# Performance work log

Measured on AMD Instinct MI355X. Metric: run time of the kernel, lower is better.

## Reference

```python
import jax, jax.numpy as jnp
import numpy as np

N, E, IN, H, C = 20000, 320000, 512, 4, 64
HC = H * C
EPS_BN = 1e-5


def setup_inputs() -> dict:
    key = jax.random.key(0)
    ks = jax.random.split(key, 12)
    p = lambda k, shape, s=0.05: jax.random.normal(k, shape, dtype=jnp.float32) * s
    z = lambda n: jnp.zeros((n,), jnp.float32)
    o = lambda n: jnp.ones((n,), jnp.float32)
    return {
        "x": jax.random.normal(ks[0], (N, IN), dtype=jnp.float32),
        "edge_index": jax.random.randint(ks[1], (2, E), 0, N),
        "Wl0": p(ks[2], (IN, HC)), "Wr0": p(ks[3], (IN, HC)),
        "att0": p(ks[4], (H, C)), "b0": z(HC),
        "g0": o(HC), "be0": z(HC), "m0": z(HC), "v0": o(HC),
        "Wl1": p(ks[5], (HC, HC)), "Wr1": p(ks[6], (HC, HC)),
        "att1": p(ks[7], (H, C)), "b1": z(HC),
        "g1": o(HC), "be1": z(HC), "m1": z(HC), "v1": o(HC),
        "Wl2": p(ks[8], (HC, 2)), "Wr2": p(ks[9], (HC, 2)),
        "att2": p(ks[10], (1, 2)), "b2": z(2),
    }


def gatv2_conv(x, Wl, Wr, att, b, ei, concat):
    # GATv2: e_ij = att . LeakyReLU(Wl x_j + Wr x_i); softmax over in-edges of i
    n = x.shape[0]
    h, c = att.shape
    xl = (x @ Wl).reshape(n, h, c)  # source/message transform
    xr = (x @ Wr).reshape(n, h, c)  # target transform
    src, dst = ei[0], ei[1]
    m = xl[src] + xr[dst]                                   # [E,H,C] edge gather
    e = jnp.sum(jax.nn.leaky_relu(m, 0.2) * att, axis=-1)   # [E,H]
    emax = jax.ops.segment_max(e, dst, num_segments=n)      # segment softmax
    emax = jnp.where(jnp.isfinite(emax), emax, 0.0)
    ex = jnp.exp(e - emax[dst])
    denom = jax.ops.segment_sum(ex, dst, num_segments=n)
    alpha = ex / (denom[dst] + 1e-16)                       # [E,H]
    out = jax.ops.segment_sum(alpha[:, :, None] * xl[src], dst, num_segments=n)
    out = out.reshape(n, h * c) if concat else out.mean(axis=1)
    return out + b


def bn_eval(x, g, be, m, v):
    return (x - m) * (g * jax.lax.rsqrt(v + EPS_BN)) + be


def reference(x, edge_index, Wl0, Wr0, att0, b0, g0, be0, m0, v0,
              Wl1, Wr1, att1, b1, g1, be1, m1, v1, Wl2, Wr2, att2, b2):
    loops = jnp.arange(N)
    ei = jnp.concatenate([edge_index, jnp.stack([loops, loops])], axis=1)
    h = gatv2_conv(x, Wl0, Wr0, att0, b0, ei, True)
    h = jax.nn.elu(bn_eval(h, g0, be0, m0, v0))
    h = gatv2_conv(h, Wl1, Wr1, att1, b1, ei, True)
    h = jax.nn.elu(bn_eval(h, g1, be1, m1, v1))
    out = gatv2_conv(h, Wl2, Wr2, att2, b2, ei, False)
    return jax.nn.log_softmax(out, axis=1)
```

## Files before the change

kernel.cpp:

```cpp
#include <hip/hip_runtime.h>
#include <math.h>

#define NN 20000
#define MP 20096
#define EE 320000
#define ET (EE + NN)
#define HC 256
#define EPS_BN 1e-5f

typedef __bf16 bf16x8 __attribute__((ext_vector_type(8)));
typedef float f32x4 __attribute__((ext_vector_type(4)));

__device__ __forceinline__ float4 ld4(const float* p) { return *reinterpret_cast<const float4*>(p); }
__device__ __forceinline__ float lrelu(float x) { return fmaxf(x, 0.f) + 0.2f * fminf(x, 0.f); }

__device__ __forceinline__ unsigned short f2b(float f) {
  unsigned int u = __float_as_uint(f);
  u = (u + 0x7fffu + ((u >> 16) & 1u)) >> 16;
  return (unsigned short)u;
}
__device__ __forceinline__ float b2f(unsigned short u) {
  return __uint_as_float(((unsigned int)u) << 16);
}

__device__ __forceinline__ void gld_lds16(const void* g, void* l) {
  __builtin_amdgcn_global_load_lds(
      (const __attribute__((address_space(1))) unsigned int*)g,
      (__attribute__((address_space(3))) unsigned int*)(unsigned int)(unsigned long long)l,
      16, 0, 0);
}

__global__ __launch_bounds__(256) void convert_x_kernel(const float* __restrict__ x,
                                                        unsigned short* __restrict__ xb) {
  int i = (blockIdx.x * 256 + threadIdx.x) * 4;
  if (i >= NN * 512) return;
  float4 v = ld4(&x[i]);
  ushort4 o;
  o.x = f2b(v.x); o.y = f2b(v.y); o.z = f2b(v.z); o.w = f2b(v.w);
  *reinterpret_cast<ushort4*>(&xb[i]) = o;
}

__global__ __launch_bounds__(256) void convert_w_kernel(const float* __restrict__ Wl,
                                                        const float* __restrict__ Wr,
                                                        unsigned short* __restrict__ Wf,
                                                        int K) {
  int idx = blockIdx.x * 256 + threadIdx.x;
  if (idx >= 512 * K) return;
  int n = idx / K, k = idx - n * K;
  float v = (n < 256) ? Wl[(size_t)k * 256 + n] : Wr[(size_t)k * 256 + (n - 256)];
  Wf[idx] = f2b(v);
}

__global__ __launch_bounds__(256) void gemm_mfma(const unsigned short* __restrict__ A,
                                                 const unsigned short* __restrict__ Bt,
                                                 unsigned short* __restrict__ xlb,
                                                 float* __restrict__ xrf,
                                                 int M, int K) {
  __shared__ unsigned short As[128 * 32];
  __shared__ unsigned short Bs[128 * 32];
  const int wave = threadIdx.x >> 6;
  const int lane = threadIdx.x & 63;
  const int am = lane & 15;
  const int aq = lane >> 4;
  const int wr = (wave >> 1) * 64;
  const int wc = (wave & 1) * 64;
  const int row0 = blockIdx.y * 128;
  const int col0 = blockIdx.x * 128;

  f32x4 acc[4][4] = {};

  for (int kk = 0; kk < K; kk += 32) {
    __syncthreads();
#pragma unroll
    for (int c = 0; c < 2; ++c) {
      int seg = wave * 128 + c * 64 + lane;
      int r = seg >> 2, ks = (seg & 3) * 8;
      gld_lds16(A + (size_t)(row0 + r) * K + kk + ks, &As[(wave * 128 + c * 64) * 8]);
      gld_lds16(Bt + (size_t)(col0 + r) * K + kk + ks, &Bs[(wave * 128 + c * 64) * 8]);
    }
    __syncthreads();

    bf16x8 af[4], bfr[4];
#pragma unroll
    for (int i = 0; i < 4; ++i)
      af[i] = *reinterpret_cast<const bf16x8*>(&As[(wr + i * 16 + am) * 32 + aq * 8]);
#pragma unroll
    for (int j = 0; j < 4; ++j)
      bfr[j] = *reinterpret_cast<const bf16x8*>(&Bs[(wc + j * 16 + am) * 32 + aq * 8]);
#pragma unroll
    for (int i = 0; i < 4; ++i)
#pragma unroll
      for (int j = 0; j < 4; ++j)
        acc[i][j] = __builtin_amdgcn_mfma_f32_16x16x32_bf16(af[i], bfr[j], acc[i][j], 0, 0, 0);
  }

#pragma unroll
  for (int i = 0; i < 4; ++i) {
#pragma unroll
    for (int j = 0; j < 4; ++j) {
      int gcol = col0 + wc + j * 16 + am;
#pragma unroll
      for (int rr = 0; rr < 4; ++rr) {
        int grow = row0 + wr + i * 16 + aq * 4 + rr;
        if (grow < M) {
          float v = acc[i][j][rr];
          if (gcol < 256) xlb[(size_t)grow * 256 + gcol] = f2b(v);
          else            xrf[(size_t)grow * 256 + (gcol - 256)] = v;
        }
      }
    }
  }
}

__global__ __launch_bounds__(256) void hist_kernel(const int* __restrict__ ei,
                                                   int* __restrict__ counts) {
  int e = blockIdx.x * blockDim.x + threadIdx.x;
  if (e >= ET) return;
  int d = (e < EE) ? ei[EE + e] : (e - EE);
  atomicAdd(&counts[d], 1);
}

__global__ __launch_bounds__(1024) void scan_kernel(int* __restrict__ cursor,
                                                    int* __restrict__ offsets) {
  __shared__ int wsum[16];
  const int tid = threadIdx.x;
  const int lane = tid & 63, wv = tid >> 6;
  const int base = tid * 20;
  int vals[20];
  int s = 0;
  if (tid < 1000) {
#pragma unroll
    for (int j = 0; j < 20; ++j) { vals[j] = cursor[base + j]; s += vals[j]; }
  }
  int ssum = s;
#pragma unroll
  for (int off = 1; off < 64; off <<= 1) {
    int t = __shfl_up(ssum, off);
    if (lane >= off) ssum += t;
  }
  if (lane == 63) wsum[wv] = ssum;
  __syncthreads();
  if (wv == 0) {
    int w = (lane < 16) ? wsum[lane] : 0;
#pragma unroll
    for (int off = 1; off < 16; off <<= 1) {
      int t = __shfl_up(w, off);
      if (lane >= off) w += t;
    }
    if (lane < 16) wsum[lane] = w;
  }
  __syncthreads();
  int excl = ssum - s + (wv > 0 ? wsum[wv - 1] : 0);
  if (tid < 1000) {
    int run = excl;
#pragma unroll
    for (int j = 0; j < 20; ++j) { offsets[base + j] = run; cursor[base + j] = run; run += vals[j]; }
  }
  if (tid == 1023) offsets[NN] = wsum[15];
}

__global__ __launch_bounds__(256) void scatter_kernel(const int* __restrict__ ei,
                                                      int* __restrict__ cursor,
                                                      int* __restrict__ srcs) {
  int e = blockIdx.x * blockDim.x + threadIdx.x;
  if (e >= ET) return;
  int s, d;
  if (e < EE) { s = ei[e]; d = ei[EE + e]; } else { s = d = e - EE; }
  int pos = atomicAdd(&cursor[d], 1);
  srcs[pos] = s;
}

__global__ __launch_bounds__(256) void gat_layer(const unsigned short* __restrict__ xlb,
                                                 const float* __restrict__ xrf,
                                                 const float* __restrict__ att,
                                                 const float* __restrict__ bias,
                                                 const float* __restrict__ gam,
                                                 const float* __restrict__ bet,
                                                 const float* __restrict__ mean,
                                                 const float* __restrict__ var,
                                                 const int* __restrict__ offsets,
                                                 const int* __restrict__ srcs,
                                                 unsigned short* __restrict__ hb) {
  const int wave = threadIdx.x >> 6;
  const int lane = threadIdx.x & 63;
  const int node = blockIdx.x * 4 + wave;
  if (node >= NN) return;

  const float4 xr4 = ld4(&xrf[(size_t)node * HC + lane * 4]);
  const float4 a4 = ld4(&att[lane * 4]);
  const int beg = offsets[node];
  const int end = offsets[node + 1];

  float lA = 0.f, lB = 0.f;
  float4 OA = make_float4(0.f, 0.f, 0.f, 0.f);
  float4 OB = make_float4(0.f, 0.f, 0.f, 0.f);

  int i = beg;
  for (; i + 3 < end; i += 4) {
    int s0 = srcs[i], s1 = srcs[i + 1], s2 = srcs[i + 2], s3 = srcs[i + 3];
    ushort4 u0 = *reinterpret_cast<const ushort4*>(&xlb[(size_t)s0 * HC + lane * 4]);
    ushort4 u1 = *reinterpret_cast<const ushort4*>(&xlb[(size_t)s1 * HC + lane * 4]);
    ushort4 u2 = *reinterpret_cast<const ushort4*>(&xlb[(size_t)s2 * HC + lane * 4]);
    ushort4 u3 = *reinterpret_cast<const ushort4*>(&xlb[(size_t)s3 * HC + lane * 4]);
    float4 x0 = make_float4(b2f(u0.x), b2f(u0.y), b2f(u0.z), b2f(u0.w));
    float4 x1 = make_float4(b2f(u1.x), b2f(u1.y), b2f(u1.z), b2f(u1.w));
    float4 x2 = make_float4(b2f(u2.x), b2f(u2.y), b2f(u2.z), b2f(u2.w));
    float4 x3 = make_float4(b2f(u3.x), b2f(u3.y), b2f(u3.z), b2f(u3.w));
    float e0 = lrelu(x0.x + xr4.x) * a4.x + lrelu(x0.y + xr4.y) * a4.y +
               lrelu(x0.z + xr4.z) * a4.z + lrelu(x0.w + xr4.w) * a4.w;
    float e1 = lrelu(x1.x + xr4.x) * a4.x + lrelu(x1.y + xr4.y) * a4.y +
               lrelu(x1.z + xr4.z) * a4.z + lrelu(x1.w + xr4.w) * a4.w;
    float e2 = lrelu(x2.x + xr4.x) * a4.x + lrelu(x2.y + xr4.y) * a4.y +
               lrelu(x2.z + xr4.z) * a4.z + lrelu(x2.w + xr4.w) * a4.w;
    float e3 = lrelu(x3.x + xr4.x) * a4.x + lrelu(x3.y + xr4.y) * a4.y +
               lrelu(x3.z + xr4.z) * a4.z + lrelu(x3.w + xr4.w) * a4.w;
#pragma unroll
    for (int off = 1; off < 16; off <<= 1) {
      e0 += __shfl_xor(e0, off);
      e1 += __shfl_xor(e1, off);
      e2 += __shfl_xor(e2, off);
      e3 += __shfl_xor(e3, off);
    }
    float p0 = __expf(e0), p1 = __expf(e1), p2 = __expf(e2), p3 = __expf(e3);
    lA += p0; lB += p1; lA += p2; lB += p3;
    OA.x += p0 * x0.x; OA.y += p0 * x0.y; OA.z += p0 * x0.z; OA.w += p0 * x0.w;
    OB.x += p1 * x1.x; OB.y += p1 * x1.y; OB.z += p1 * x1.z; OB.w += p1 * x1.w;
    OA.x += p2 * x2.x; OA.y += p2 * x2.y; OA.z += p2 * x2.z; OA.w += p2 * x2.w;
    OB.x += p3 * x3.x; OB.y += p3 * x3.y; OB.z += p3 * x3.z; OB.w += p3 * x3.w;
  }
  for (; i < end; ++i) {
    int s = srcs[i];
    ushort4 u = *reinterpret_cast<const ushort4*>(&xlb[(size_t)s * HC + lane * 4]);
    float4 x0 = make_float4(b2f(u.x), b2f(u.y), b2f(u.z), b2f(u.w));
    float e = lrelu(x0.x + xr4.x) * a4.x + lrelu(x0.y + xr4.y) * a4.y +
              lrelu(x0.z + xr4.z) * a4.z + lrelu(x0.w + xr4.w) * a4.w;
#pragma unroll
    for (int off = 1; off < 16; off <<= 1) e += __shfl_xor(e, off);
    float p = __expf(e);
    lA += p;
    OA.x += p * x0.x; OA.y += p * x0.y; OA.z += p * x0.z; OA.w += p * x0.w;
  }
  float inv = 1.f / (lA + lB);
  float4 O = make_float4(OA.x + OB.x, OA.y + OB.y, OA.z + OB.z, OA.w + OB.w);

  float4 b4 = ld4(&bias[lane * 4]);
  float4 g4 = ld4(&gam[lane * 4]);
  float4 e4 = ld4(&bet[lane * 4]);
  float4 m4 = ld4(&mean[lane * 4]);
  float4 v4 = ld4(&var[lane * 4]);
  float y0 = O.x * inv + b4.x, y1 = O.y * inv + b4.y;
  float y2 = O.z * inv + b4.z, y3 = O.w * inv + b4.w;
  float z0 = (y0 - m4.x) * (g4.x * rsqrtf(v4.x + EPS_BN)) + e4.x;
  float z1 = (y1 - m4.y) * (g4.y * rsqrtf(v4.y + EPS_BN)) + e4.y;
  float z2 = (y2 - m4.z) * (g4.z * rsqrtf(v4.z + EPS_BN)) + e4.z;
  float z3 = (y3 - m4.w) * (g4.w * rsqrtf(v4.w + EPS_BN)) + e4.w;
  ushort4 r;
  r.x = f2b(z0 > 0.f ? z0 : expm1f(z0));
  r.y = f2b(z1 > 0.f ? z1 : expm1f(z1));
  r.z = f2b(z2 > 0.f ? z2 : expm1f(z2));
  r.w = f2b(z3 > 0.f ? z3 : expm1f(z3));
  *reinterpret_cast<ushort4*>(&hb[(size_t)node * HC + lane * 4]) = r;
}

__global__ __launch_bounds__(256) void lin2_kernel(const unsigned short* __restrict__ hb,
                                                   const float* __restrict__ Wl,
                                                   const float* __restrict__ Wr,
                                                   float* __restrict__ xl2,
                                                   float* __restrict__ xr2) {
  const int wave = threadIdx.x >> 6;
  const int lane = threadIdx.x & 63;
  const int node = blockIdx.x * 4 + wave;
  if (node >= NN) return;
  ushort4 h4 = *reinterpret_cast<const ushort4*>(&hb[(size_t)node * HC + lane * 4]);
  float hv[4] = {b2f(h4.x), b2f(h4.y), b2f(h4.z), b2f(h4.w)};
  float l0 = 0.f, l1 = 0.f, r0 = 0.f, r1 = 0.f;
#pragma unroll
  for (int j = 0; j < 4; ++j) {
    int row = lane * 4 + j;
    l0 += hv[j] * Wl[row * 2 + 0];
    l1 += hv[j] * Wl[row * 2 + 1];
    r0 += hv[j] * Wr[row * 2 + 0];
    r1 += hv[j] * Wr[row * 2 + 1];
  }
#pragma unroll
  for (int off = 1; off < 64; off <<= 1) {
    l0 += __shfl_xor(l0, off);
    l1 += __shfl_xor(l1, off);
    r0 += __shfl_xor(r0, off);
    r1 += __shfl_xor(r1, off);
  }
  if (lane == 0) {
    xl2[node * 2 + 0] = l0; xl2[node * 2 + 1] = l1;
    xr2[node * 2 + 0] = r0; xr2[node * 2 + 1] = r1;
  }
}

__global__ __launch_bounds__(256) void gat2_out_kernel(const float* __restrict__ xl2,
                                                       const float* __restrict__ xr2,
                                                       const float* __restrict__ att2,
                                                       const float* __restrict__ b2,
                                                       const int* __restrict__ offsets,
                                                       const int* __restrict__ srcs,
                                                       float* __restrict__ out) {
  const int wave = threadIdx.x >> 6;
  const int lane = threadIdx.x & 63;
  const int node = blockIdx.x * 4 + wave;
  if (node >= NN) return;
  const float a0 = att2[0], a1 = att2[1];
  const float xr0 = xr2[node * 2 + 0], xr1 = xr2[node * 2 + 1];
  const int beg = offsets[node], end = offsets[node + 1];

  float l = 0.f, o0 = 0.f, o1 = 0.f;
  for (int i = beg + lane; i < end; i += 64) {
    int s = srcs[i];
    float x0 = xl2[s * 2 + 0], x1 = xl2[s * 2 + 1];
    float e = lrelu(x0 + xr0) * a0 + lrelu(x1 + xr1) * a1;
    float p = __expf(e);
    l += p;
    o0 += p * x0;
    o1 += p * x1;
  }
#pragma unroll
  for (int off = 1; off < 64; off <<= 1) {
    l += __shfl_xor(l, off);
    o0 += __shfl_xor(o0, off);
    o1 += __shfl_xor(o1, off);
  }
  if (lane == 0) {
    float inv = 1.f / l;
    float t0 = o0 * inv + b2[0];
    float t1 = o1 * inv + b2[1];
    float mx = fmaxf(t0, t1);
    float ls = mx + logf(__expf(t0 - mx) + __expf(t1 - mx));
    out[node * 2 + 0] = t0 - ls;
    out[node * 2 + 1] = t1 - ls;
  }
}

extern "C" void kernel_launch(void* const* d_in, const int* in_sizes, int n_in,
                              void* d_out, int out_size, void* d_ws, size_t ws_size,
                              hipStream_t stream) {
  const float* x    = (const float*)d_in[0];
  const int*   ei   = (const int*)d_in[1];
  const float* Wl0  = (const float*)d_in[2];
  const float* Wr0  = (const float*)d_in[3];
  const float* att0 = (const float*)d_in[4];
  const float* b0   = (const float*)d_in[5];
  const float* g0   = (const float*)d_in[6];
  const float* be0  = (const float*)d_in[7];
  const float* m0   = (const float*)d_in[8];
  const float* v0   = (const float*)d_in[9];
  const float* Wl1  = (const float*)d_in[10];
  const float* Wr1  = (const float*)d_in[11];
  const float* att1 = (const float*)d_in[12];
  const float* b1   = (const float*)d_in[13];
  const float* g1   = (const float*)d_in[14];
  const float* be1  = (const float*)d_in[15];
  const float* m1   = (const float*)d_in[16];
  const float* v1   = (const float*)d_in[17];
  const float* Wl2  = (const float*)d_in[18];
  const float* Wr2  = (const float*)d_in[19];
  const float* att2 = (const float*)d_in[20];
  const float* b2   = (const float*)d_in[21];

  float* xrf = (float*)d_ws;
  unsigned short* xlb = (unsigned short*)(xrf + (size_t)NN * 256);
  unsigned short* hb  = xlb + (size_t)NN * 256;
  unsigned short* xb  = hb + (size_t)MP * 256;
  unsigned short* Wf0 = xb + (size_t)MP * 512;
  unsigned short* Wf1 = Wf0 + 512 * 512;
  float* xl2 = (float*)(Wf1 + 512 * 256);
  float* xr2 = xl2 + 2 * NN;
  int* offsets = (int*)(xr2 + 2 * NN);
  int* cursor  = offsets + (NN + 1);
  int* srcs    = cursor + NN;

  hipMemsetAsync(cursor, 0, NN * sizeof(int), stream);
  hist_kernel<<<(ET + 255) / 256, 256, 0, stream>>>(ei, cursor);
  convert_x_kernel<<<(NN * 512 / 4 + 255) / 256, 256, 0, stream>>>(x, xb);
  convert_w_kernel<<<(512 * 512 + 255) / 256, 256, 0, stream>>>(Wl0, Wr0, Wf0, 512);
  convert_w_kernel<<<(512 * 256 + 255) / 256, 256, 0, stream>>>(Wl1, Wr1, Wf1, 256);
  scan_kernel<<<1, 1024, 0, stream>>>(cursor, offsets);
  scatter_kernel<<<(ET + 255) / 256, 256, 0, stream>>>(ei, cursor, srcs);

  dim3 gemm_grid(4, MP / 128);
  gemm_mfma<<<gemm_grid, 256, 0, stream>>>(xb, Wf0, xlb, xrf, NN, 512);
  gat_layer<<<NN / 4, 256, 0, stream>>>(xlb, xrf, att0, b0, g0, be0, m0, v0, offsets, srcs, hb);
  gemm_mfma<<<gemm_grid, 256, 0, stream>>>(hb, Wf1, xlb, xrf, NN, 256);
  gat_layer<<<NN / 4, 256, 0, stream>>>(xlb, xrf, att1, b1, g1, be1, m1, v1, offsets, srcs, hb);
  lin2_kernel<<<NN / 4, 256, 0, stream>>>(hb, Wl2, Wr2, xl2, xr2);
  gat2_out_kernel<<<NN / 4, 256, 0, stream>>>(xl2, xr2, att2, b2, offsets, srcs, (float*)d_out);
}
```

Before: 301.6 us.

## Fuse prep kernels, split GAT edges across two waves, fuse lin2 into layer1

Merges the x conversion, both weight conversions and the degree histogram into one launch. The GAT layers now assign two waves per node, each handling half the in-edges, and merge partial sums through shared memory. The final projection (lin2) is folded into the second GAT layer's epilogue, so the hidden activations are no longer written out and read back. The aim is fewer launches, more parallelism for latency-bound gathers, and less memory traffic, at the cost of a block barrier and an idle second wave during the epilogue.

```diff
diff --git a/kernel.cpp b/kernel.cpp
--- a/kernel.cpp
+++ b/kernel.cpp
@@ -8,6 +8,12 @@
 #define HC 256
 #define EPS_BN 1e-5f
 
+#define PB_CX 5000
+#define PB_W0 1024
+#define PB_W1 512
+#define PB_HIST 1329
+#define PB_TOTAL (PB_CX + PB_W0 + PB_W1 + PB_HIST)
+
 typedef __bf16 bf16x8 __attribute__((ext_vector_type(8)));
 typedef float f32x4 __attribute__((ext_vector_type(4)));
 
@@ -30,25 +36,44 @@
       16, 0, 0);
 }
 
-__global__ __launch_bounds__(256) void convert_x_kernel(const float* __restrict__ x,
-                                                        unsigned short* __restrict__ xb) {
-  int i = (blockIdx.x * 256 + threadIdx.x) * 4;
-  if (i >= NN * 512) return;
-  float4 v = ld4(&x[i]);
-  ushort4 o;
-  o.x = f2b(v.x); o.y = f2b(v.y); o.z = f2b(v.z); o.w = f2b(v.w);
-  *reinterpret_cast<ushort4*>(&xb[i]) = o;
-}
-
-__global__ __launch_bounds__(256) void convert_w_kernel(const float* __restrict__ Wl,
-                                                        const float* __restrict__ Wr,
-                                                        unsigned short* __restrict__ Wf,
-                                                        int K) {
-  int idx = blockIdx.x * 256 + threadIdx.x;
-  if (idx >= 512 * K) return;
-  int n = idx / K, k = idx - n * K;
-  float v = (n < 256) ? Wl[(size_t)k * 256 + n] : Wr[(size_t)k * 256 + (n - 256)];
-  Wf[idx] = f2b(v);
+__global__ __launch_bounds__(256) void prep_kernel(const float* __restrict__ x,
+                                                   unsigned short* __restrict__ xb,
+                                                   const float* __restrict__ Wl0,
+                                                   const float* __restrict__ Wr0,
+                                                   unsigned short* __restrict__ Wf0,
+                                                   const float* __restrict__ Wl1,
+                                                   const float* __restrict__ Wr1,
+                                                   unsigned short* __restrict__ Wf1,
+                                                   const int* __restrict__ ei,
+                                                   int* __restrict__ counts) {
+  const int b = blockIdx.x;
+  const int tid = threadIdx.x;
+  if (b < PB_CX) {
+    int i = (b * 256 + tid) * 8;
+    float4 v0 = ld4(&x[i]);
+    float4 v1 = ld4(&x[i + 4]);
+    ushort4 o0, o1;
+    o0.x = f2b(v0.x); o0.y = f2b(v0.y); o0.z = f2b(v0.z); o0.w = f2b(v0.w);
+    o1.x = f2b(v1.x); o1.y = f2b(v1.y); o1.z = f2b(v1.z); o1.w = f2b(v1.w);
+    *reinterpret_cast<ushort4*>(&xb[i]) = o0;
+    *reinterpret_cast<ushort4*>(&xb[i + 4]) = o1;
+  } else if (b < PB_CX + PB_W0) {
+    int idx = (b - PB_CX) * 256 + tid;
+    int n = idx >> 9, k = idx & 511;
+    float v = (n < 256) ? Wl0[(size_t)k * 256 + n] : Wr0[(size_t)k * 256 + (n - 256)];
+    Wf0[idx] = f2b(v);
+  } else if (b < PB_CX + PB_W0 + PB_W1) {
+    int idx = (b - PB_CX - PB_W0) * 256 + tid;
+    int n = idx >> 8, k = idx & 255;
+    float v = (n < 256) ? Wl1[(size_t)k * 256 + n] : Wr1[(size_t)k * 256 + (n - 256)];
+    Wf1[idx] = f2b(v);
+  } else {
+    int e = (b - PB_CX - PB_W0 - PB_W1) * 256 + tid;
+    if (e < ET) {
+      int d = (e < EE) ? ei[EE + e] : (e - EE);
+      atomicAdd(&counts[d], 1);
+    }
+  }
 }
 
 __global__ __launch_bounds__(256) void gemm_mfma(const unsigned short* __restrict__ A,
@@ -112,14 +137,6 @@
   }
 }
 
-__global__ __launch_bounds__(256) void hist_kernel(const int* __restrict__ ei,
-                                                   int* __restrict__ counts) {
-  int e = blockIdx.x * blockDim.x + threadIdx.x;
-  if (e >= ET) return;
-  int d = (e < EE) ? ei[EE + e] : (e - EE);
-  atomicAdd(&counts[d], 1);
-}
-
 __global__ __launch_bounds__(1024) void scan_kernel(int* __restrict__ cursor,
                                                     int* __restrict__ offsets) {
   __shared__ int wsum[16];
@@ -170,31 +187,14 @@
   srcs[pos] = s;
 }
 
-__global__ __launch_bounds__(256) void gat_layer(const unsigned short* __restrict__ xlb,
-                                                 const float* __restrict__ xrf,
-                                                 const float* __restrict__ att,
-                                                 const float* __restrict__ bias,
-                                                 const float* __restrict__ gam,
-                                                 const float* __restrict__ bet,
-                                                 const float* __restrict__ mean,
-                                                 const float* __restrict__ var,
-                                                 const int* __restrict__ offsets,
-                                                 const int* __restrict__ srcs,
-                                                 unsigned short* __restrict__ hb) {
-  const int wave = threadIdx.x >> 6;
-  const int lane = threadIdx.x & 63;
-  const int node = blockIdx.x * 4 + wave;
-  if (node >= NN) return;
-
-  const float4 xr4 = ld4(&xrf[(size_t)node * HC + lane * 4]);
-  const float4 a4 = ld4(&att[lane * 4]);
-  const int beg = offsets[node];
-  const int end = offsets[node + 1];
-
+__device__ __forceinline__ void gat_accum(const unsigned short* __restrict__ xlb,
+                                          const int* __restrict__ srcs,
+                                          int beg, int end, int lane,
+                                          float4 xr4, float4 a4,
+                                          float& lsum, float4& O) {
   float lA = 0.f, lB = 0.f;
   float4 OA = make_float4(0.f, 0.f, 0.f, 0.f);
   float4 OB = make_float4(0.f, 0.f, 0.f, 0.f);
-
   int i = beg;
   for (; i + 3 < end; i += 4) {
     int s0 = srcs[i], s1 = srcs[i + 1], s2 = srcs[i + 2], s3 = srcs[i + 3];
@@ -240,58 +240,109 @@
     lA += p;
     OA.x += p * x0.x; OA.y += p * x0.y; OA.z += p * x0.z; OA.w += p * x0.w;
   }
-  float inv = 1.f / (lA + lB);
-  float4 O = make_float4(OA.x + OB.x, OA.y + OB.y, OA.z + OB.z, OA.w + OB.w);
-
-  float4 b4 = ld4(&bias[lane * 4]);
-  float4 g4 = ld4(&gam[lane * 4]);
-  float4 e4 = ld4(&bet[lane * 4]);
-  float4 m4 = ld4(&mean[lane * 4]);
-  float4 v4 = ld4(&var[lane * 4]);
-  float y0 = O.x * inv + b4.x, y1 = O.y * inv + b4.y;
-  float y2 = O.z * inv + b4.z, y3 = O.w * inv + b4.w;
-  float z0 = (y0 - m4.x) * (g4.x * rsqrtf(v4.x + EPS_BN)) + e4.x;
-  float z1 = (y1 - m4.y) * (g4.y * rsqrtf(v4.y + EPS_BN)) + e4.y;
-  float z2 = (y2 - m4.z) * (g4.z * rsqrtf(v4.z + EPS_BN)) + e4.z;
-  float z3 = (y3 - m4.w) * (g4.w * rsqrtf(v4.w + EPS_BN)) + e4.w;
-  ushort4 r;
-  r.x = f2b(z0 > 0.f ? z0 : expm1f(z0));
-  r.y = f2b(z1 > 0.f ? z1 : expm1f(z1));
-  r.z = f2b(z2 > 0.f ? z2 : expm1f(z2));
-  r.w = f2b(z3 > 0.f ? z3 : expm1f(z3));
-  *reinterpret_cast<ushort4*>(&hb[(size_t)node * HC + lane * 4]) = r;
-}
-
-__global__ __launch_bounds__(256) void lin2_kernel(const unsigned short* __restrict__ hb,
-                                                   const float* __restrict__ Wl,
-                                                   const float* __restrict__ Wr,
-                                                   float* __restrict__ xl2,
-                                                   float* __restrict__ xr2) {
-  const int wave = threadIdx.x >> 6;
-  const int lane = threadIdx.x & 63;
-  const int node = blockIdx.x * 4 + wave;
-  if (node >= NN) return;
-  ushort4 h4 = *reinterpret_cast<const ushort4*>(&hb[(size_t)node * HC + lane * 4]);
-  float hv[4] = {b2f(h4.x), b2f(h4.y), b2f(h4.z), b2f(h4.w)};
-  float l0 = 0.f, l1 = 0.f, r0 = 0.f, r1 = 0.f;
-#pragma unroll
-  for (int j = 0; j < 4; ++j) {
-    int row = lane * 4 + j;
-    l0 += hv[j] * Wl[row * 2 + 0];
-    l1 += hv[j] * Wl[row * 2 + 1];
-    r0 += hv[j] * Wr[row * 2 + 0];
-    r1 += hv[j] * Wr[row * 2 + 1];
-  }
-#pragma unroll
-  for (int off = 1; off < 64; off <<= 1) {
-    l0 += __shfl_xor(l0, off);
-    l1 += __shfl_xor(l1, off);
-    r0 += __shfl_xor(r0, off);
-    r1 += __shfl_xor(r1, off);
-  }
-  if (lane == 0) {
-    xl2[node * 2 + 0] = l0; xl2[node * 2 + 1] = l1;
-    xr2[node * 2 + 0] = r0; xr2[node * 2 + 1] = r1;
+  lsum = lA + lB;
+  O = make_float4(OA.x + OB.x, OA.y + OB.y, OA.z + OB.z, OA.w + OB.w);
+}
+
+#define GAT2W_PROLOG                                                         \
+  const int wave = threadIdx.x >> 6;                                         \
+  const int lane = threadIdx.x & 63;                                         \
+  const int team = wave >> 1;                                                \
+  const int wt = wave & 1;                                                   \
+  const int node = blockIdx.x * 2 + team;                                    \
+  const float4 xr4 = ld4(&xrf[(size_t)node * HC + lane * 4]);                \
+  const float4 a4 = ld4(&att[lane * 4]);                                     \
+  const int beg0 = offsets[node];                                            \
+  const int end0 = offsets[node + 1];                                        \
+  const int deg = end0 - beg0;                                               \
+  const int h = min(deg, ((deg + 7) >> 3) << 2);                             \
+  const int beg = wt ? beg0 + h : beg0;                                      \
+  const int end = wt ? end0 : beg0 + h;                                      \
+  float lsum; float4 O;                                                      \
+  gat_accum(xlb, srcs, beg, end, lane, xr4, a4, lsum, O);                    \
+  if (wt == 1) {                                                             \
+    float* m = &mrg[team][lane][0];                                          \
+    m[0] = lsum; m[1] = O.x; m[2] = O.y; m[3] = O.z; m[4] = O.w;             \
+  }                                                                          \
+  __syncthreads();
+
+#define GAT2W_MERGE_BN                                                       \
+  const float* m = &mrg[team][lane][0];                                      \
+  lsum += m[0]; O.x += m[1]; O.y += m[2]; O.z += m[3]; O.w += m[4];          \
+  float inv = 1.f / lsum;                                                    \
+  float4 b4 = ld4(&bias[lane * 4]);                                          \
+  float4 g4 = ld4(&gam[lane * 4]);                                           \
+  float4 e4 = ld4(&bet[lane * 4]);                                           \
+  float4 m4 = ld4(&mean[lane * 4]);                                          \
+  float4 v4 = ld4(&var[lane * 4]);                                           \
+  float z0 = (O.x * inv + b4.x - m4.x) * (g4.x * rsqrtf(v4.x + EPS_BN)) + e4.x; \
+  float z1 = (O.y * inv + b4.y - m4.y) * (g4.y * rsqrtf(v4.y + EPS_BN)) + e4.y; \
+  float z2 = (O.z * inv + b4.z - m4.z) * (g4.z * rsqrtf(v4.z + EPS_BN)) + e4.z; \
+  float z3 = (O.w * inv + b4.w - m4.w) * (g4.w * rsqrtf(v4.w + EPS_BN)) + e4.w; \
+  z0 = (z0 > 0.f) ? z0 : expm1f(z0);                                         \
+  z1 = (z1 > 0.f) ? z1 : expm1f(z1);                                         \
+  z2 = (z2 > 0.f) ? z2 : expm1f(z2);                                         \
+  z3 = (z3 > 0.f) ? z3 : expm1f(z3);
+
+__global__ __launch_bounds__(256) void gat_layer0(const unsigned short* __restrict__ xlb,
+                                                  const float* __restrict__ xrf,
+                                                  const float* __restrict__ att,
+                                                  const float* __restrict__ bias,
+                                                  const float* __restrict__ gam,
+                                                  const float* __restrict__ bet,
+                                                  const float* __restrict__ mean,
+                                                  const float* __restrict__ var,
+                                                  const int* __restrict__ offsets,
+                                                  const int* __restrict__ srcs,
+                                                  unsigned short* __restrict__ hb) {
+  __shared__ float mrg[2][64][5];
+  GAT2W_PROLOG
+  if (wt == 0) {
+    GAT2W_MERGE_BN
+    ushort4 r;
+    r.x = f2b(z0); r.y = f2b(z1); r.z = f2b(z2); r.w = f2b(z3);
+    *reinterpret_cast<ushort4*>(&hb[(size_t)node * HC + lane * 4]) = r;
+  }
+}
+
+__global__ __launch_bounds__(256) void gat_layer1(const unsigned short* __restrict__ xlb,
+                                                  const float* __restrict__ xrf,
+                                                  const float* __restrict__ att,
+                                                  const float* __restrict__ bias,
+                                                  const float* __restrict__ gam,
+                                                  const float* __restrict__ bet,
+                                                  const float* __restrict__ mean,
+                                                  const float* __restrict__ var,
+                                                  const int* __restrict__ offsets,
+                                                  const int* __restrict__ srcs,
+                                                  const float* __restrict__ Wl2,
+                                                  const float* __restrict__ Wr2,
+                                                  float* __restrict__ xl2,
+                                                  float* __restrict__ xr2) {
+  __shared__ float mrg[2][64][5];
+  GAT2W_PROLOG
+  if (wt == 0) {
+    GAT2W_MERGE_BN
+    const int row = lane * 4;
+    float4 wlA = ld4(&Wl2[row * 2]);
+    float4 wlB = ld4(&Wl2[row * 2 + 4]);
+    float4 wrA = ld4(&Wr2[row * 2]);
+    float4 wrB = ld4(&Wr2[row * 2 + 4]);
+    float pl0 = z0 * wlA.x + z1 * wlA.z + z2 * wlB.x + z3 * wlB.z;
+    float pl1 = z0 * wlA.y + z1 * wlA.w + z2 * wlB.y + z3 * wlB.w;
+    float pr0 = z0 * wrA.x + z1 * wrA.z + z2 * wrB.x + z3 * wrB.z;
+    float pr1 = z0 * wrA.y + z1 * wrA.w + z2 * wrB.y + z3 * wrB.w;
+#pragma unroll
+    for (int off = 1; off < 64; off <<= 1) {
+      pl0 += __shfl_xor(pl0, off);
+      pl1 += __shfl_xor(pl1, off);
+      pr0 += __shfl_xor(pr0, off);
+      pr1 += __shfl_xor(pr1, off);
+    }
+    if (lane == 0) {
+      xl2[node * 2 + 0] = pl0; xl2[node * 2 + 1] = pl1;
+      xr2[node * 2 + 0] = pr0; xr2[node * 2 + 1] = pr1;
+    }
   }
 }
 
@@ -376,18 +427,15 @@
   int* srcs    = cursor + NN;
 
   hipMemsetAsync(cursor, 0, NN * sizeof(int), stream);
-  hist_kernel<<<(ET + 255) / 256, 256, 0, stream>>>(ei, cursor);
-  convert_x_kernel<<<(NN * 512 / 4 + 255) / 256, 256, 0, stream>>>(x, xb);
-  convert_w_kernel<<<(512 * 512 + 255) / 256, 256, 0, stream>>>(Wl0, Wr0, Wf0, 512);
-  convert_w_kernel<<<(512 * 256 + 255) / 256, 256, 0, stream>>>(Wl1, Wr1, Wf1, 256);
+  prep_kernel<<<PB_TOTAL, 256, 0, stream>>>(x, xb, Wl0, Wr0, Wf0, Wl1, Wr1, Wf1, ei, cursor);
   scan_kernel<<<1, 1024, 0, stream>>>(cursor, offsets);
   scatter_kernel<<<(ET + 255) / 256, 256, 0, stream>>>(ei, cursor, srcs);
 
   dim3 gemm_grid(4, MP / 128);
   gemm_mfma<<<gemm_grid, 256, 0, stream>>>(xb, Wf0, xlb, xrf, NN, 512);
-  gat_layer<<<NN / 4, 256, 0, stream>>>(xlb, xrf, att0, b0, g0, be0, m0, v0, offsets, srcs, hb);
+  gat_layer0<<<NN / 2, 256, 0, stream>>>(xlb, xrf, att0, b0, g0, be0, m0, v0, offsets, srcs, hb);
   gemm_mfma<<<gemm_grid, 256, 0, stream>>>(hb, Wf1, xlb, xrf, NN, 256);
-  gat_layer<<<NN / 4, 256, 0, stream>>>(xlb, xrf, att1, b1, g1, be1, m1, v1, offsets, srcs, hb);
-  lin2_kernel<<<NN / 4, 256, 0, stream>>>(hb, Wl2, Wr2, xl2, xr2);
+  gat_layer1<<<NN / 2, 256, 0, stream>>>(xlb, xrf, att1, b1, g1, be1, m1, v1, offsets, srcs,
+                                         Wl2, Wr2, xl2, xr2);
   gat2_out_kernel<<<NN / 4, 256, 0, stream>>>(xl2, xr2, att2, b2, offsets, srcs, (float*)d_out);
 }
```

After: 302.3 us. No clear change (+0.2%).
